# Kernel optimization log

Hardware: AMD Instinct MI355X
Metric: run time of the kernel (lower is better)

The kernel has to match this reference:

```python
import jax, jax.numpy as jnp
import numpy as np

B, T, D, H = 64, 1024, 512, 512
_SCALE = 1.0 / np.sqrt(H)  # torch-style RNNCell init scale


def setup_inputs() -> dict:
    key = jax.random.key(0)
    ks = jax.random.split(key, 9)
    f32 = jnp.float32
    return {
        "x": jax.random.normal(ks[0], (B, T, D), dtype=f32),
        "Wih_f": jax.random.normal(ks[1], (H, D), dtype=f32) * _SCALE,
        "Whh_f": jax.random.normal(ks[2], (H, H), dtype=f32) * _SCALE,
        "bih_f": jax.random.normal(ks[3], (H,), dtype=f32) * _SCALE,
        "bhh_f": jax.random.normal(ks[4], (H,), dtype=f32) * _SCALE,
        "Wih_b": jax.random.normal(ks[5], (H, D), dtype=f32) * _SCALE,
        "Whh_b": jax.random.normal(ks[6], (H, H), dtype=f32) * _SCALE,
        "bih_b": jax.random.normal(ks[7], (H,), dtype=f32) * _SCALE,
        "bhh_b": jax.random.normal(ks[8], (H,), dtype=f32) * _SCALE,
    }


def _scan_direction(x_bt, Wih, Whh, bih, bhh):
    # x_bt: [B, T, D] already in processing order for this direction.
    # Precompute the input projection for all timesteps (one big GEMM),
    # leaving only the recurrent GEMM inside the scan.
    xp = jnp.einsum('btd,hd->bth', x_bt, Wih) + bih + bhh  # [B, T, H]
    h0 = jnp.zeros((x_bt.shape[0], Whh.shape[0]), dtype=x_bt.dtype)

    def step(h, xt):  # xt: [B, H]
        h_new = jnp.tanh(xt + h @ Whh.T)
        return h_new, h_new

    _, hs = jax.lax.scan(step, h0, jnp.swapaxes(xp, 0, 1))  # hs: [T, B, H]
    return jnp.swapaxes(hs, 0, 1)  # [B, T, H] in processing order


def reference(x, Wih_f, Whh_f, bih_f, bhh_f, Wih_b, Whh_b, bih_b, bhh_b):
    # Forward direction: timesteps 0..T-1.
    fh = _scan_direction(x, Wih_f, Whh_f, bih_f, bhh_f)
    # Backward direction: cell consumes x reversed in time; torch code appends
    # hiddens in processing order (i.e., index t <-> original time T-1-t).
    bh = _scan_direction(x[:, ::-1, :], Wih_b, Whh_b, bih_b, bhh_b)
    # output_last=False branch: [B, 2, T, H]
    return jnp.stack([fh, bh], axis=1)
```

## Files before the change

kernel.cpp:

```cpp
#include <hip/hip_runtime.h>
#include <hip/hip_fp16.h>
#include <cstdint>

typedef _Float16 h2 __attribute__((ext_vector_type(2)));
typedef _Float16 h8 __attribute__((ext_vector_type(8)));
typedef float    f4 __attribute__((ext_vector_type(4)));
typedef uint32_t u4 __attribute__((ext_vector_type(4)));

#define BATCH 64
#define TSTEPS 1024
#define DDIM 512
#define HDIM 512

static __device__ __forceinline__ float fdot2(uint32_t w, uint32_t h, float acc) {
  return __builtin_amdgcn_fdot2(__builtin_bit_cast(h2, w), __builtin_bit_cast(h2, h), acc, false);
}

#define BAR_LDS()                                            \
  do {                                                       \
    __builtin_amdgcn_sched_barrier(0);                       \
    asm volatile("s_waitcnt lgkmcnt(0)" ::: "memory");       \
    __builtin_amdgcn_s_barrier();                            \
    __builtin_amdgcn_sched_barrier(0);                       \
  } while (0)

__global__ void prep_kernel(const float* __restrict__ Wih_f, const float* __restrict__ Whh_f,
                            const float* __restrict__ bih_f, const float* __restrict__ bhh_f,
                            const float* __restrict__ Wih_b, const float* __restrict__ Whh_b,
                            const float* __restrict__ bih_b, const float* __restrict__ bhh_b,
                            _Float16* __restrict__ wi16, uint32_t* __restrict__ whT,
                            float* __restrict__ bsum) {
  int i = blockIdx.x * 256 + threadIdx.x;
  if (i < 2 * 512 * 512) {
    const float* s = (i < 512 * 512) ? Wih_f : Wih_b;
    wi16[i] = (_Float16)s[i & (512 * 512 - 1)];
  }
  if (i < 2 * 256 * 512) {
    int d = i >> 17; int rem = i & ((1 << 17) - 1);
    int kp = rem >> 9; int j = rem & 511;
    const float* W = d ? Whh_b : Whh_f;
    h2 p; p[0] = (_Float16)W[j * 512 + 2 * kp]; p[1] = (_Float16)W[j * 512 + 2 * kp + 1];
    whT[i] = __builtin_bit_cast(uint32_t, p);
  }
  if (i < 2 * 512) {
    int d = i >> 9, j = i & 511;
    bsum[i] = d ? (bih_b[j] + bhh_b[j]) : (bih_f[j] + bhh_f[j]);
  }
}

__global__ __launch_bounds__(256) void xp_gemm(const float* __restrict__ x,
                                               const _Float16* __restrict__ wi,
                                               const float* __restrict__ bsum,
                                               _Float16* __restrict__ xp) {
  __shared__ _Float16 As[128][40];
  __shared__ _Float16 Bs[128][40];
  const int mt = blockIdx.x, nt = blockIdx.y, dir = blockIdx.z;
  const int m0 = mt * 128, n0 = nt * 128;
  const int tid = threadIdx.x;
  const int lane = tid & 63, w = tid >> 6;
  const int wr = w >> 1, wc = w & 1;
  const int ra = tid >> 1, hf = tid & 1;

  const int mrow = m0 + ra;
  const int bb = mrow >> 10, pp = mrow & 1023;
  const int srow = dir ? ((bb << 10) + (1023 - pp)) : mrow;
  const float*    xbase = x + (size_t)srow * 512 + hf * 16;
  const _Float16* wbase = wi + (size_t)dir * 512 * 512 + (size_t)(n0 + ra) * 512 + hf * 16;

  f4 acc[4][4];
  #pragma unroll
  for (int a = 0; a < 4; ++a)
    #pragma unroll
    for (int b = 0; b < 4; ++b) acc[a][b] = (f4)0.f;

  for (int k0 = 0; k0 < 512; k0 += 32) {
    f4 x0 = *(const f4*)(xbase + k0);
    f4 x1 = *(const f4*)(xbase + k0 + 4);
    f4 x2 = *(const f4*)(xbase + k0 + 8);
    f4 x3 = *(const f4*)(xbase + k0 + 12);
    h8 b0 = *(const h8*)(wbase + k0);
    h8 b1 = *(const h8*)(wbase + k0 + 8);
    h8 a0, a1;
    #pragma unroll
    for (int u = 0; u < 4; ++u) {
      a0[u] = (_Float16)x0[u]; a0[4 + u] = (_Float16)x1[u];
      a1[u] = (_Float16)x2[u]; a1[4 + u] = (_Float16)x3[u];
    }
    __syncthreads();
    *(h8*)&As[ra][hf * 16]     = a0;
    *(h8*)&As[ra][hf * 16 + 8] = a1;
    *(h8*)&Bs[ra][hf * 16]     = b0;
    *(h8*)&Bs[ra][hf * 16 + 8] = b1;
    __syncthreads();
    h8 af[4], bf[4];
    #pragma unroll
    for (int fm = 0; fm < 4; ++fm)
      af[fm] = *(const h8*)&As[wr * 64 + fm * 16 + (lane & 15)][(lane >> 4) * 8];
    #pragma unroll
    for (int fn = 0; fn < 4; ++fn)
      bf[fn] = *(const h8*)&Bs[wc * 64 + fn * 16 + (lane & 15)][(lane >> 4) * 8];
    #pragma unroll
    for (int fm = 0; fm < 4; ++fm)
      #pragma unroll
      for (int fn = 0; fn < 4; ++fn)
        acc[fm][fn] = __builtin_amdgcn_mfma_f32_16x16x32_f16(af[fm], bf[fn], acc[fm][fn], 0, 0, 0);
  }

  float bsv[4];
  #pragma unroll
  for (int fn = 0; fn < 4; ++fn)
    bsv[fn] = bsum[dir * 512 + n0 + wc * 64 + fn * 16 + (lane & 15)];
  #pragma unroll
  for (int fm = 0; fm < 4; ++fm)
    #pragma unroll
    for (int fn = 0; fn < 4; ++fn)
      #pragma unroll
      for (int u = 0; u < 4; ++u) {
        int m = m0 + wr * 64 + fm * 16 + (lane >> 4) * 4 + u;
        int n = n0 + wc * 64 + fn * 16 + (lane & 15);
        xp[((size_t)dir << 25) + (size_t)m * 512 + n] = (_Float16)(acc[fm][fn][u] + bsv[fn]);
      }
}

__global__ __launch_bounds__(1024, 4) void rnn_rec(const _Float16* __restrict__ xp,
                                                   const uint32_t* __restrict__ whT,
                                                   float* __restrict__ out) {
  extern __shared__ char smem[];
  uint32_t* wl   = (uint32_t*)smem;
  uint32_t* hl   = (uint32_t*)(smem + 131072);
  float*    psum = (float*)(smem + 132096);

  const int bid = blockIdx.x;
  const int dir = bid & 1, b = bid >> 1;
  const int l = threadIdx.x;
  const int q = l >> 8, r = l & 255;

  const uint32_t* wb = whT + dir * (256 * 512) + (q * 64) * 512 + r;
  uint32_t w0[64], w1[32];
  #pragma unroll
  for (int p = 0; p < 64; ++p) w0[p] = wb[p * 512];
  #pragma unroll
  for (int p = 0; p < 32; ++p) w1[p] = wb[p * 512 + 256];

  char* wlb = (char*)wl + (l >> 3) * 1024 + (l & 7) * 16;
  #pragma unroll
  for (int g = 0; g < 8; ++g) {
    u4 v;
    #pragma unroll
    for (int i = 0; i < 4; ++i) v[i] = wb[(32 + g * 4 + i) * 512 + 256];
    *(u4*)(wlb + g * 128) = v;
  }
  if (l < 256) hl[l] = 0;
  __syncthreads();

  const _Float16* xpp = xp + ((size_t)dir << 25) + ((size_t)b << 19);
  float* op = out + (((size_t)(b * 2 + dir)) << 19);

  for (int t = 0; t < TSTEPS; ++t) {
    float xpv = 0.f;
    if (l < 512) xpv = (float)xpp[(size_t)t * 512 + l];

    float acc0 = 0.f, acc1 = 0.f;
    const uint32_t* hq = hl + q * 64;
    #pragma unroll
    for (int cb = 0; cb < 16; ++cb) {
      u4 hv = *(const u4*)(hq + cb * 4);
      if (cb < 8) {
        #pragma unroll
        for (int i = 0; i < 4; ++i) {
          acc0 = fdot2(w0[cb * 4 + i], hv[i], acc0);
          acc1 = fdot2(w1[cb * 4 + i], hv[i], acc1);
        }
      } else {
        u4 wv = *(const u4*)(wlb + (cb - 8) * 128);
        #pragma unroll
        for (int i = 0; i < 4; ++i) {
          acc0 = fdot2(w0[cb * 4 + i], hv[i], acc0);
          acc1 = fdot2(wv[i], hv[i], acc1);
        }
      }
    }
    psum[q * 520 + r]       = acc0;
    psum[q * 520 + 256 + r] = acc1;
    BAR_LDS();

    if (l < 512) {
      float s = psum[l] + psum[520 + l] + psum[1040 + l] + psum[1560 + l] + xpv;
      float e = __expf(2.f * s);
      float hv = 1.f - 2.f * __builtin_amdgcn_rcpf(e + 1.f);
      op[(size_t)t * 512 + l] = hv;
      ((_Float16*)hl)[l] = (_Float16)hv;
    }
    BAR_LDS();
  }
}

extern "C" void kernel_launch(void* const* d_in, const int* in_sizes, int n_in,
                              void* d_out, int out_size, void* d_ws, size_t ws_size,
                              hipStream_t stream) {
  const float* x     = (const float*)d_in[0];
  const float* Wih_f = (const float*)d_in[1];
  const float* Whh_f = (const float*)d_in[2];
  const float* bih_f = (const float*)d_in[3];
  const float* bhh_f = (const float*)d_in[4];
  const float* Wih_b = (const float*)d_in[5];
  const float* Whh_b = (const float*)d_in[6];
  const float* bih_b = (const float*)d_in[7];
  const float* bhh_b = (const float*)d_in[8];

  char* ws = (char*)d_ws;
  _Float16* xp16 = (_Float16*)ws;
  _Float16* wi16 = (_Float16*)(ws + 134217728);
  uint32_t* whT  = (uint32_t*)(ws + 135266304);
  float*    bsum = (float*)(ws + 136314880);
  float* out = (float*)d_out;

  prep_kernel<<<2048, 256, 0, stream>>>(Wih_f, Whh_f, bih_f, bhh_f,
                                        Wih_b, Whh_b, bih_b, bhh_b, wi16, whT, bsum);
  dim3 g(512, 4, 2);
  xp_gemm<<<g, 256, 0, stream>>>(x, wi16, bsum, xp16);

  const int REC_LDS = 140416;
  hipFuncSetAttribute((const void*)rnn_rec, hipFuncAttributeMaxDynamicSharedMemorySize, REC_LDS);
  rnn_rec<<<128, 1024, REC_LDS, stream>>>(xp16, whT, out);
}
```

Measured before the change: 1.568 ms.

## Repartition recurrent matvec so each lane owns four outputs, broadcasting h via readlane

The recurrent step is restructured. Each wave now covers a 32-pair slice of k and each lane computes four adjacent output columns, so weights load as u4 vectors. The hidden state is read once per lane from LDS and broadcast to scalar registers with readlane, replacing the repeated vector LDS reads of h. The aim is lower LDS traffic and fewer register weights per output column. In exchange there are eight partial sums per output instead of four, which means a larger psum buffer and more adds in the tanh stage, plus 32 readlanes on every step.

```diff
diff --git a/kernel.cpp b/kernel.cpp
--- a/kernel.cpp
+++ b/kernel.cpp
@@ -133,23 +133,20 @@
   const int bid = blockIdx.x;
   const int dir = bid & 1, b = bid >> 1;
   const int l = threadIdx.x;
-  const int q = l >> 8, r = l & 255;
-
-  const uint32_t* wb = whT + dir * (256 * 512) + (q * 64) * 512 + r;
-  uint32_t w0[64], w1[32];
-  #pragma unroll
-  for (int p = 0; p < 64; ++p) w0[p] = wb[p * 512];
-  #pragma unroll
-  for (int p = 0; p < 32; ++p) w1[p] = wb[p * 512 + 256];
+  const int w = l >> 6, lv = l & 63;
+  const int ke = w >> 1, jh = w & 1;
+  const int jbase = jh * 256 + lv * 4;
+
+  const uint32_t* wb = whT + dir * (256 * 512) + (ke * 32) * 512 + jbase;
+  u4 wr_[24];
+  #pragma unroll
+  for (int p = 0; p < 24; ++p) wr_[p] = *(const u4*)(wb + p * 512);
 
   char* wlb = (char*)wl + (l >> 3) * 1024 + (l & 7) * 16;
   #pragma unroll
-  for (int g = 0; g < 8; ++g) {
-    u4 v;
-    #pragma unroll
-    for (int i = 0; i < 4; ++i) v[i] = wb[(32 + g * 4 + i) * 512 + 256];
-    *(u4*)(wlb + g * 128) = v;
-  }
+  for (int g = 0; g < 8; ++g)
+    *(u4*)(wlb + g * 128) = *(const u4*)(wb + (24 + g) * 512);
+
   if (l < 256) hl[l] = 0;
   __syncthreads();
 
@@ -160,32 +157,32 @@
     float xpv = 0.f;
     if (l < 512) xpv = (float)xpp[(size_t)t * 512 + l];
 
-    float acc0 = 0.f, acc1 = 0.f;
-    const uint32_t* hq = hl + q * 64;
-    #pragma unroll
-    for (int cb = 0; cb < 16; ++cb) {
-      u4 hv = *(const u4*)(hq + cb * 4);
-      if (cb < 8) {
-        #pragma unroll
-        for (int i = 0; i < 4; ++i) {
-          acc0 = fdot2(w0[cb * 4 + i], hv[i], acc0);
-          acc1 = fdot2(w1[cb * 4 + i], hv[i], acc1);
-        }
-      } else {
-        u4 wv = *(const u4*)(wlb + (cb - 8) * 128);
-        #pragma unroll
-        for (int i = 0; i < 4; ++i) {
-          acc0 = fdot2(w0[cb * 4 + i], hv[i], acc0);
-          acc1 = fdot2(wv[i], hv[i], acc1);
-        }
-      }
-    }
-    psum[q * 520 + r]       = acc0;
-    psum[q * 520 + 256 + r] = acc1;
+    uint32_t hvl = hl[ke * 32 + (lv & 31)];
+    uint32_t hs[32];
+    #pragma unroll
+    for (int p = 0; p < 32; ++p) hs[p] = __builtin_amdgcn_readlane(hvl, p);
+
+    f4 acc = (f4)0.f;
+    #pragma unroll
+    for (int p = 0; p < 24; ++p) {
+      #pragma unroll
+      for (int i = 0; i < 4; ++i) acc[i] = fdot2(wr_[p][i], hs[p], acc[i]);
+    }
+    #pragma unroll
+    for (int g = 0; g < 8; ++g) {
+      u4 wv = *(const u4*)(wlb + g * 128);
+      #pragma unroll
+      for (int i = 0; i < 4; ++i) acc[i] = fdot2(wv[i], hs[24 + g], acc[i]);
+    }
+    *(f4*)&psum[ke * 512 + jbase] = acc;
     BAR_LDS();
 
     if (l < 512) {
-      float s = psum[l] + psum[520 + l] + psum[1040 + l] + psum[1560 + l] + xpv;
+      float s0 = psum[l]          + psum[512 + l];
+      float s1 = psum[1024 + l]   + psum[1536 + l];
+      float s2 = psum[2048 + l]   + psum[2560 + l];
+      float s3 = psum[3072 + l]   + psum[3584 + l];
+      float s = ((s0 + s1) + (s2 + s3)) + xpv;
       float e = __expf(2.f * s);
       float hv = 1.f - 2.f * __builtin_amdgcn_rcpf(e + 1.f);
       op[(size_t)t * 512 + l] = hv;
@@ -220,7 +217,7 @@
   dim3 g(512, 4, 2);
   xp_gemm<<<g, 256, 0, stream>>>(x, wi16, bsum, xp16);
 
-  const int REC_LDS = 140416;
+  const int REC_LDS = 148480;
   hipFuncSetAttribute((const void*)rnn_rec, hipFuncAttributeMaxDynamicSharedMemorySize, REC_LDS);
   rnn_rec<<<128, 1024, REC_LDS, stream>>>(xp16, whT, out);
 }
```

Measured after the change: 1.742 ms. 11.1% more time.

## Restructure recurrent kernel to 512 threads with shuffle reduction and single barrier

Applied to the files above, without the earlier changes.

The recurrent kernel now runs 512 threads per block. Each thread computes 4 output columns over a 128-wide K slice, with 208 fp16 pairs held in registers and 48 in LDS. The K-partial sums are combined with cross-lane shuffles instead of an LDS psum array, and the hidden state is double-buffered so each timestep needs one barrier instead of two. The aim is to cut per-step synchronisation and LDS traffic on the serial critical path. In exchange, register pressure rises sharply (52 u4 weight vectors) and the tanh is computed redundantly by 4 lanes per output.

```diff
diff --git a/kernel.cpp b/kernel.cpp
--- a/kernel.cpp
+++ b/kernel.cpp
@@ -4,6 +4,7 @@
 
 typedef _Float16 h2 __attribute__((ext_vector_type(2)));
 typedef _Float16 h8 __attribute__((ext_vector_type(8)));
+typedef float    f2 __attribute__((ext_vector_type(2)));
 typedef float    f4 __attribute__((ext_vector_type(4)));
 typedef uint32_t u4 __attribute__((ext_vector_type(4)));
 
@@ -122,75 +123,97 @@
       }
 }
 
-__global__ __launch_bounds__(1024, 4) void rnn_rec(const _Float16* __restrict__ xp,
-                                                   const uint32_t* __restrict__ whT,
-                                                   float* __restrict__ out) {
+__global__ __launch_bounds__(512, 2) void rnn_rec(const _Float16* __restrict__ xp,
+                                                  const uint32_t* __restrict__ whT,
+                                                  float* __restrict__ out) {
   extern __shared__ char smem[];
-  uint32_t* wl   = (uint32_t*)smem;
-  uint32_t* hl   = (uint32_t*)(smem + 131072);
-  float*    psum = (float*)(smem + 132096);
+  uint32_t* wl = (uint32_t*)smem;
+  char* hbase  = smem + 98304;
 
   const int bid = blockIdx.x;
   const int dir = bid & 1, b = bid >> 1;
   const int l = threadIdx.x;
-  const int q = l >> 8, r = l & 255;
-
-  const uint32_t* wb = whT + dir * (256 * 512) + (q * 64) * 512 + r;
-  uint32_t w0[64], w1[32];
-  #pragma unroll
-  for (int p = 0; p < 64; ++p) w0[p] = wb[p * 512];
-  #pragma unroll
-  for (int p = 0; p < 32; ++p) w1[p] = wb[p * 512 + 256];
-
-  char* wlb = (char*)wl + (l >> 3) * 1024 + (l & 7) * 16;
-  #pragma unroll
-  for (int g = 0; g < 8; ++g) {
-    u4 v;
-    #pragma unroll
-    for (int i = 0; i < 4; ++i) v[i] = wb[(32 + g * 4 + i) * 512 + 256];
-    *(u4*)(wlb + g * 128) = v;
-  }
-  if (l < 256) hl[l] = 0;
+  const int wj = l >> 6, lv = l & 63;
+  const int kq = lv >> 4, jj = lv & 15;
+  const int jq0 = wj * 64 + jj * 4;
+
+  const uint32_t* wb = whT + dir * (256 * 512) + (kq * 64) * 512 + jq0;
+  u4 wq[52];
+  #pragma unroll
+  for (int p = 0; p < 52; ++p) wq[p] = *(const u4*)(wb + p * 512);
+
+  char* wlb = (char*)wl + (l >> 3) * 1536 + (l & 7) * 16;
+  #pragma unroll
+  for (int g = 0; g < 12; ++g)
+    *(u4*)(wlb + g * 128) = *(const u4*)(wb + (52 + g) * 512);
+
+  {
+    uint32_t* hz = (uint32_t*)hbase;
+    for (int i = l; i < 2080; i += 512) hz[i] = 0;
+  }
   __syncthreads();
 
   const _Float16* xpp = xp + ((size_t)dir << 25) + ((size_t)b << 19);
   float* op = out + (((size_t)(b * 2 + dir)) << 19);
 
+  const int hrd_off = kq * 1296;
+  const int hwr_off = kq * 1040 + wj * 128 + jj * 8;
+
   for (int t = 0; t < TSTEPS; ++t) {
-    float xpv = 0.f;
-    if (l < 512) xpv = (float)xpp[(size_t)t * 512 + l];
-
-    float acc0 = 0.f, acc1 = 0.f;
-    const uint32_t* hq = hl + q * 64;
-    #pragma unroll
-    for (int cb = 0; cb < 16; ++cb) {
-      u4 hv = *(const u4*)(hq + cb * 4);
-      if (cb < 8) {
+    uint2 xv = *(const uint2*)(xpp + (size_t)t * 512 + jq0);
+
+    const char* hrd = hbase + (t & 1) * 4160 + hrd_off;
+    f4 acc = (f4)0.f;
+
+    #pragma unroll
+    for (int cb = 0; cb < 13; ++cb) {
+      u4 hv = *(const u4*)(hrd + cb * 16);
+      #pragma unroll
+      for (int i = 0; i < 4; ++i) {
+        const int p = cb * 4 + i;
         #pragma unroll
-        for (int i = 0; i < 4; ++i) {
-          acc0 = fdot2(w0[cb * 4 + i], hv[i], acc0);
-          acc1 = fdot2(w1[cb * 4 + i], hv[i], acc1);
-        }
-      } else {
-        u4 wv = *(const u4*)(wlb + (cb - 8) * 128);
+        for (int jn = 0; jn < 4; ++jn) acc[jn] = fdot2(wq[p][jn], hv[i], acc[jn]);
+      }
+    }
+    #pragma unroll
+    for (int cb2 = 0; cb2 < 3; ++cb2) {
+      u4 hv = *(const u4*)(hrd + (13 + cb2) * 16);
+      #pragma unroll
+      for (int i = 0; i < 4; ++i) {
+        u4 wv = *(const u4*)(wlb + (cb2 * 4 + i) * 128);
         #pragma unroll
-        for (int i = 0; i < 4; ++i) {
-          acc0 = fdot2(w0[cb * 4 + i], hv[i], acc0);
-          acc1 = fdot2(wv[i], hv[i], acc1);
-        }
+        for (int jn = 0; jn < 4; ++jn) acc[jn] = fdot2(wv[jn], hv[i], acc[jn]);
       }
     }
-    psum[q * 520 + r]       = acc0;
-    psum[q * 520 + 256 + r] = acc1;
-    BAR_LDS();
-
-    if (l < 512) {
-      float s = psum[l] + psum[520 + l] + psum[1040 + l] + psum[1560 + l] + xpv;
-      float e = __expf(2.f * s);
-      float hv = 1.f - 2.f * __builtin_amdgcn_rcpf(e + 1.f);
-      op[(size_t)t * 512 + l] = hv;
-      ((_Float16*)hl)[l] = (_Float16)hv;
-    }
+
+    #pragma unroll
+    for (int jn = 0; jn < 4; ++jn) acc[jn] += __shfl_xor(acc[jn], 16, 64);
+    #pragma unroll
+    for (int jn = 0; jn < 4; ++jn) acc[jn] += __shfl_xor(acc[jn], 32, 64);
+
+    h2 x01 = __builtin_bit_cast(h2, xv.x);
+    h2 x23 = __builtin_bit_cast(h2, xv.y);
+    float s0 = acc[0] + (float)x01[0];
+    float s1 = acc[1] + (float)x01[1];
+    float s2 = acc[2] + (float)x23[0];
+    float s3 = acc[3] + (float)x23[1];
+    float h0 = 1.f - 2.f * __builtin_amdgcn_rcpf(__expf(2.f * s0) + 1.f);
+    float h1 = 1.f - 2.f * __builtin_amdgcn_rcpf(__expf(2.f * s1) + 1.f);
+    float h2v = 1.f - 2.f * __builtin_amdgcn_rcpf(__expf(2.f * s2) + 1.f);
+    float h3 = 1.f - 2.f * __builtin_amdgcn_rcpf(__expf(2.f * s3) + 1.f);
+
+    if (kq == 0) {
+      f4 o; o[0] = h0; o[1] = h1; o[2] = h2v; o[3] = h3;
+      *(f4*)(op + (size_t)t * 512 + jq0) = o;
+    }
+
+    h2 pk0; pk0[0] = (_Float16)h0; pk0[1] = (_Float16)h1;
+    h2 pk1; pk1[0] = (_Float16)h2v; pk1[1] = (_Float16)h3;
+    uint2 hw;
+    hw.x = __builtin_bit_cast(uint32_t, pk0);
+    hw.y = __builtin_bit_cast(uint32_t, pk1);
+    *(uint2*)(hbase + ((t + 1) & 1) * 4160 + hwr_off) = hw;
+
     BAR_LDS();
   }
 }
@@ -220,7 +243,7 @@
   dim3 g(512, 4, 2);
   xp_gemm<<<g, 256, 0, stream>>>(x, wi16, bsum, xp16);
 
-  const int REC_LDS = 140416;
+  const int REC_LDS = 106624;
   hipFuncSetAttribute((const void*)rnn_rec, hipFuncAttributeMaxDynamicSharedMemorySize, REC_LDS);
-  rnn_rec<<<128, 1024, REC_LDS, stream>>>(xp16, whT, out);
-}
+  rnn_rec<<<128, 512, REC_LDS, stream>>>(xp16, whT, out);
+}
```

New measurement: 1.744 ms. 11.2% more time.
